# Optimization experiments

Measured on AMD Instinct MI355X. Metric: run time of the kernel, lower is better.

## Reference

```python
import jax, jax.numpy as jnp
import numpy as np

N, E, D, A = 50000, 1_600_000, 32, 2
H1, C1, H2, C2 = 4, 16, 2, 32  # GATv2Conv(D,16,heads=4) -> 64; GATv2Conv(64,32,heads=2) -> 64


def setup_inputs() -> dict:
    key = jax.random.key(0)
    ks = jax.random.split(key, 16)

    def glorot(k, shape):
        fan = shape[0] + shape[-1]
        return jax.random.normal(k, shape, jnp.float32) * np.float32(np.sqrt(2.0 / fan))

    return {
        "x": jax.random.normal(ks[0], (N, D), jnp.float32),
        "edge_index": jax.random.randint(ks[1], (2, E), 0, N),
        "edge_attr": jax.random.normal(ks[2], (E, 2), jnp.float32),
        # GATv2 layer 1 (lin_l/lin_r with bias, lin_edge no bias, att [H,C], out bias)
        "w1_l": glorot(ks[3], (D, H1 * C1)), "b1_l": jnp.zeros((H1 * C1,), jnp.float32),
        "w1_r": glorot(ks[4], (D, H1 * C1)), "b1_r": jnp.zeros((H1 * C1,), jnp.float32),
        "w1_e": glorot(ks[5], (2, H1 * C1)),
        "att1": glorot(ks[6], (H1, C1)),
        "bias1": jnp.zeros((H1 * C1,), jnp.float32),
        # GATv2 layer 2
        "w2_l": glorot(ks[7], (H1 * C1, H2 * C2)), "b2_l": jnp.zeros((H2 * C2,), jnp.float32),
        "w2_r": glorot(ks[8], (H1 * C1, H2 * C2)), "b2_r": jnp.zeros((H2 * C2,), jnp.float32),
        "w2_e": glorot(ks[9], (2, H2 * C2)),
        "att2": glorot(ks[10], (H2, C2)),
        "bias2": jnp.zeros((H2 * C2,), jnp.float32),
        # heads
        "w_actor": glorot(ks[11], (H2 * C2, A)), "b_actor": jnp.zeros((A,), jnp.float32),
        "w_critic": glorot(ks[12], (H2 * C2, 1)), "b_critic": jnp.zeros((1,), jnp.float32),
        "log_std": jnp.zeros((A,), jnp.float32),
    }


def _gatv2(x, src, dst, eattr, Wl, bl, Wr, br, We, att, bias, H, C, n):
    # PyG GATv2Conv: message j->i with i = dst, j = src
    xl = (x @ Wl + bl).reshape(n, H, C)  # source-side transform (x_j)
    xr = (x @ Wr + br).reshape(n, H, C)  # target-side transform (x_i)
    ee = (eattr @ We).reshape(-1, H, C)  # per-edge embedding
    z = jax.nn.leaky_relu(xl[src] + xr[dst] + ee, 0.2)  # [Etot, H, C]
    logits = jnp.einsum('ehc,hc->eh', z, att)  # [Etot, H]
    # segment softmax over incoming edges of each dst node
    m = jax.ops.segment_max(logits, dst, num_segments=n)
    p = jnp.exp(logits - m[dst])
    denom = jax.ops.segment_sum(p, dst, num_segments=n)
    alpha = p / denom[dst]  # every node has a self-loop -> denom > 0
    msg = xl[src] * alpha[:, :, None]  # [Etot, H, C]
    out = jax.ops.segment_sum(msg, dst, num_segments=n)
    return out.reshape(n, H * C) + bias


def reference(x, edge_index, edge_attr,
              w1_l, b1_l, w1_r, b1_r, w1_e, att1, bias1,
              w2_l, b2_l, w2_r, b2_r, w2_e, att2, bias2,
              w_actor, b_actor, w_critic, b_critic, log_std):
    src, dst = edge_index[0], edge_index[1]
    # add_self_loops=True, fill_value='mean': self-loop edge_attr = mean of incoming edge_attr
    cnt = jax.ops.segment_sum(jnp.ones((edge_attr.shape[0],), x.dtype), dst, num_segments=N)
    sums = jax.ops.segment_sum(edge_attr, dst, num_segments=N)
    loop_attr = sums / jnp.maximum(cnt, 1.0)[:, None]
    loop = jnp.arange(N, dtype=src.dtype)
    src_f = jnp.concatenate([src, loop])
    dst_f = jnp.concatenate([dst, loop])
    ea = jnp.concatenate([edge_attr, loop_attr], axis=0)

    h = jax.nn.relu(_gatv2(x, src_f, dst_f, ea, w1_l, b1_l, w1_r, b1_r, w1_e, att1, bias1, H1, C1, N))
    h = jax.nn.relu(_gatv2(h, src_f, dst_f, ea, w2_l, b2_l, w2_r, b2_r, w2_e, att2, bias2, H2, C2, N))

    action_mean = jnp.tanh(h @ w_actor + b_actor)  # [N, A]
    value = h @ w_critic + b_critic               # [N, 1]
    std = jnp.exp(log_std)                        # [A]  (Normal(action_mean, std))
    return action_mean, std, value
```

## Files before the change

### kernel.cpp

```cpp
#include <hip/hip_runtime.h>
#include <hip/hip_fp16.h>
#include <math.h>

#define DIN   32
#define F1    64
#define F2    64

typedef _Float16 h2 __attribute__((ext_vector_type(2)));

template <class T, class F>
__device__ __forceinline__ T bitc(F f) { return __builtin_bit_cast(T, f); }

__device__ __forceinline__ unsigned f16pack(float a, float b) {
    h2 h = { (_Float16)a, (_Float16)b };
    return bitc<unsigned>(h);
}

template <int K>
__device__ __forceinline__ void lin_lr_body(int bid,
        const float* __restrict__ x,
        const float* __restrict__ Wl, const float* __restrict__ bl,
        const float* __restrict__ Wr, const float* __restrict__ br,
        __half* __restrict__ xl, float* __restrict__ xr, int n) {
    __shared__ float Ash[32][K + 4];
    __shared__ float Wsh[K][128];
    const int t = threadIdx.x;
    const int node0 = bid * 32;

    for (int idx = t; idx < 32 * (K / 4); idx += 256) {
        int m = idx / (K / 4), kq = idx % (K / 4);
        float4 v = make_float4(0.f, 0.f, 0.f, 0.f);
        if (node0 + m < n) v = ((const float4*)(x + (size_t)(node0 + m) * K))[kq];
        *(float4*)&Ash[m][kq * 4] = v;
    }
    for (int idx = t; idx < K * 32; idx += 256) {
        int k = idx / 32, j4 = idx % 32;
        float4 v = (j4 < 16) ? ((const float4*)(Wl + (size_t)k * 64))[j4]
                             : ((const float4*)(Wr + (size_t)k * 64))[j4 - 16];
        *(float4*)&Wsh[k][j4 * 4] = v;
    }
    __syncthreads();

    const int ty = t >> 4;
    const int tx = t & 15;
    float acc0[8], acc1[8];
#pragma unroll
    for (int j = 0; j < 8; j++) { acc0[j] = 0.f; acc1[j] = 0.f; }

#pragma unroll 4
    for (int k = 0; k < K; k++) {
        float a0 = Ash[ty * 2 + 0][k];
        float a1 = Ash[ty * 2 + 1][k];
        float4 w0 = *(const float4*)&Wsh[k][tx * 8];
        float4 w1 = *(const float4*)&Wsh[k][tx * 8 + 4];
        acc0[0] += a0 * w0.x; acc0[1] += a0 * w0.y;
        acc0[2] += a0 * w0.z; acc0[3] += a0 * w0.w;
        acc0[4] += a0 * w1.x; acc0[5] += a0 * w1.y;
        acc0[6] += a0 * w1.z; acc0[7] += a0 * w1.w;
        acc1[0] += a1 * w0.x; acc1[1] += a1 * w0.y;
        acc1[2] += a1 * w0.z; acc1[3] += a1 * w0.w;
        acc1[4] += a1 * w1.x; acc1[5] += a1 * w1.y;
        acc1[6] += a1 * w1.z; acc1[7] += a1 * w1.w;
    }

    const float* bsrc = (tx < 8) ? bl : br;
    int jb = (tx < 8) ? tx * 8 : (tx - 8) * 8;
    float4 b0 = ((const float4*)(bsrc + jb))[0];
    float4 b1 = ((const float4*)(bsrc + jb))[1];
#pragma unroll
    for (int m = 0; m < 2; m++) {
        int node = node0 + ty * 2 + m;
        if (node >= n) continue;
        const float* ac = (m == 0) ? acc0 : acc1;
        float o0 = ac[0] + b0.x, o1 = ac[1] + b0.y;
        float o2 = ac[2] + b0.z, o3 = ac[3] + b0.w;
        float o4 = ac[4] + b1.x, o5 = ac[5] + b1.y;
        float o6 = ac[6] + b1.z, o7 = ac[7] + b1.w;
        if (tx < 8) {
            uint4 pk;
            pk.x = f16pack(o0, o1); pk.y = f16pack(o2, o3);
            pk.z = f16pack(o4, o5); pk.w = f16pack(o6, o7);
            *((uint4*)(xl + (size_t)node * 64 + jb)) = pk;
        } else {
            ((float4*)(xr + (size_t)node * 64 + jb))[0] = make_float4(o0, o1, o2, o3);
            ((float4*)(xr + (size_t)node * 64 + jb))[1] = make_float4(o4, o5, o6, o7);
        }
    }
}

__global__ __launch_bounds__(256, 2)
void fused_bcount_lin1(const int* __restrict__ dstr, int* __restrict__ cursor,
                       int* __restrict__ chunkoff, int* __restrict__ rank,
                       int E, int Ec, int NB, int gridLin,
                       const float* __restrict__ x,
                       const float* __restrict__ Wl, const float* __restrict__ bl,
                       const float* __restrict__ Wr, const float* __restrict__ br,
                       __half* __restrict__ xl, float* __restrict__ xr, int n) {
    __shared__ int hist[256];
    if ((int)blockIdx.x < gridLin) {
        lin_lr_body<DIN>(blockIdx.x, x, Wl, bl, Wr, br, xl, xr, n);
        return;
    }
    const int blk = blockIdx.x - gridLin;
    const int t = threadIdx.x;
    hist[t] = 0;
    __syncthreads();
    const int s0 = blk * Ec, s1 = min(E, s0 + Ec);
    for (int e = s0 + t; e < s1; e += 256)
        rank[e] = atomicAdd(&hist[dstr[e] >> 8], 1);
    __syncthreads();
    if (t < NB) {
        int h = hist[t];
        chunkoff[blk * 256 + t] = h ? atomicAdd(&cursor[t], h) : 0;
    }
}

__global__ __launch_bounds__(512)
void scatter_buckets(const int* __restrict__ srcr, const int* __restrict__ dstr,
                     const float* __restrict__ ea, const int* __restrict__ rank,
                     const int* __restrict__ chunkoff,
                     int2* __restrict__ inter, int E, int Ec, int NB, int cap) {
    __shared__ int colsh[256];
    const int blk = blockIdx.x;
    const int t = threadIdx.x;
    if (t < 256) colsh[t] = (t < NB) ? (t * cap + chunkoff[blk * 256 + t]) : 0;
    __syncthreads();
    const int s0 = blk * Ec, s1 = min(E, s0 + Ec);
    for (int e = s0 + t; e < s1; e += 512) {
        int d = dstr[e];
        float2 v = ((const float2*)ea)[e];
        int2 r;
        r.x = srcr[e] | ((d & 255) << 24);
        r.y = (int)f16pack(v.x, v.y);
        inter[colsh[d >> 8] + rank[e]] = r;
    }
}

__global__ __launch_bounds__(512)
void bucket_csr(const int2* __restrict__ inter, const int* __restrict__ cursor,
                int2* __restrict__ rse, float2* __restrict__ la2,
                int2* __restrict__ edges, int NB, int N, int cap) {
    __shared__ int sh[256];
    __shared__ int cur[256];
    const int b = blockIdx.x, t = threadIdx.x;
    const int bstart = b * cap;
    const int bend = bstart + cursor[b];

    if (t < 256) sh[t] = 0;
    __syncthreads();
    for (int pos = bstart + t; pos < bend; pos += 512)
        atomicAdd(&sh[((unsigned)inter[pos].x) >> 24], 1);
    __syncthreads();
    int cnt_v = 0, myrs = 0;
    if (t < 256) cnt_v = sh[t];
    __syncthreads();
    if (t < 256) sh[t] = cnt_v;
    __syncthreads();
    for (int off = 1; off < 256; off <<= 1) {
        int x = (t >= off && t < 256) ? sh[t - off] : 0;
        __syncthreads();
        if (t < 256) sh[t] += x;
        __syncthreads();
    }
    if (t < 256) {
        int excl = sh[t] - cnt_v;
        cur[t] = excl;
        myrs = bstart + excl;
        int node = b * 256 + t;
        if (node < N) rse[node] = make_int2(myrs, myrs + cnt_v);
    }
    __syncthreads();
    for (int pos = bstart + t; pos < bend; pos += 512) {
        int2 r = inter[pos];
        int k = atomicAdd(&cur[((unsigned)r.x) >> 24], 1);
        r.x &= 0x00FFFFFF;
        edges[bstart + k] = r;
    }
    int zend = (b + 1) * cap + ((b == NB - 1) ? 64 : 0);
    for (int pos = bend + t; pos < zend; pos += 512)
        edges[pos] = make_int2(0, 0);
    __syncthreads();
    if (t < 256) {
        int node = b * 256 + t;
        if (node < N) {
            float s0 = 0.f, s1 = 0.f;
            for (int pos = myrs; pos < myrs + cnt_v; pos++) {
                unsigned u = (unsigned)edges[pos].y;
                s0 += (float)bitc<_Float16>((unsigned short)(u & 0xFFFFu));
                s1 += (float)bitc<_Float16>((unsigned short)(u >> 16));
            }
            float inv = cnt_v ? 1.0f / (float)cnt_v : 0.f;
            la2[node] = make_float2(s0 * inv, s1 * inv);
        }
    }
}

__global__ __launch_bounds__(256, 2)
void lin_lr_tiled64(const float* __restrict__ x,
                    const float* __restrict__ Wl, const float* __restrict__ bl,
                    const float* __restrict__ Wr, const float* __restrict__ br,
                    __half* __restrict__ xl, float* __restrict__ xr, int n) {
    lin_lr_body<F1>(blockIdx.x, x, Wl, bl, Wr, br, xl, xr, n);
}

template <int H, int C, bool FUSE_HEADS>
__global__ __launch_bounds__(256)
void gat_kernel(const __half* __restrict__ xl, const float* __restrict__ xr,
                const int2* __restrict__ rse, const float2* __restrict__ la2,
                const int2* __restrict__ edges,
                const float* __restrict__ We, const float* __restrict__ att,
                const float* __restrict__ bias, float* __restrict__ hout,
                const float* __restrict__ wa, const float* __restrict__ ba,
                const float* __restrict__ wc, const float* __restrict__ bcv,
                const float* __restrict__ ls, float* __restrict__ pout,
                int n) {
    constexpr int LPH = C / 4;
    if (FUSE_HEADS && blockIdx.x == 0 && threadIdx.x < 2)
        pout[(size_t)n * 2 + threadIdx.x] = expf(ls[threadIdx.x]);
    const int lane = threadIdx.x & 63;
    const int wid = (blockIdx.x * blockDim.x + threadIdx.x) >> 6;
    if (wid >= n) return;
    const int i = wid;
    const int g = lane >> 4;
    const int q = lane & 15;

    const uint2* xlh = (const uint2*)xl;
    const float4 xri = ((const float4*)(xr + (size_t)i * 64))[q];
    const float4 we0 = ((const float4*)We)[q];
    const float4 we1 = ((const float4*)(We + 64))[q];
    float4 av = ((const float4*)att)[q];
    const float LOG2E = 1.4426950408889634f;
    av.x *= LOG2E; av.y *= LOG2E; av.z *= LOG2E; av.w *= LOG2E;

    const h2 xrih01 = { (_Float16)xri.x, (_Float16)xri.y };
    const h2 xrih23 = { (_Float16)xri.z, (_Float16)xri.w };
    const h2 we0h01 = { (_Float16)we0.x, (_Float16)we0.y };
    const h2 we0h23 = { (_Float16)we0.z, (_Float16)we0.w };
    const h2 we1h01 = { (_Float16)we1.x, (_Float16)we1.y };
    const h2 we1h23 = { (_Float16)we1.z, (_Float16)we1.w };
    const h2 avh01  = { (_Float16)av.x, (_Float16)av.y };
    const h2 avh23  = { (_Float16)av.z, (_Float16)av.w };
    const h2 lk = { (_Float16)0.2f, (_Float16)0.2f };

    float den = 0.f;
    float a0 = 0.f, a1 = 0.f, a2 = 0.f, a3 = 0.f;

    const int2 se = rse[i];
    const int e0 = se.x, e1 = se.y;
    const int r = (e1 - e0) & 7;

    auto edge_logit = [&](unsigned eabits, uint2 xp, float2& f01, float2& f23) -> float {
        h2 ea0h = bitc<h2>((eabits & 0xFFFFu) | (eabits << 16));
        h2 ea1h = bitc<h2>((eabits >> 16) | (eabits & 0xFFFF0000u));
        h2 xv01 = bitc<h2>(xp.x), xv23 = bitc<h2>(xp.y);
        h2 z01 = xv01 + (ea0h * we0h01 + (ea1h * we1h01 + xrih01));
        h2 z23 = xv23 + (ea0h * we0h23 + (ea1h * we1h23 + xrih23));
        z01 = __builtin_elementwise_max(z01, z01 * lk);
        z23 = __builtin_elementwise_max(z23, z23 * lk);
        f01 = make_float2((float)xv01[0], (float)xv01[1]);
        f23 = make_float2((float)xv23[0], (float)xv23[1]);
        return __builtin_amdgcn_fdot2(z01, avh01,
               __builtin_amdgcn_fdot2(z23, avh23, 0.f, false), false);
    };

    if (r) {
        int2 h0 = edges[e0 + g];
        int2 h1 = edges[e0 + 4 + g];
        uint2 xp0 = xlh[(h0.x << 4) + q];
        uint2 xp1 = xlh[(h1.x << 4) + q];
        const bool v0 = g < r;
        const bool v1 = (4 + g) < r;
        float2 f001, f023, f101, f123;
        float l0 = edge_logit((unsigned)h0.y, xp0, f001, f023);
        float l1 = edge_logit((unsigned)h1.y, xp1, f101, f123);
#pragma unroll
        for (int m = 1; m < LPH; m <<= 1) {
            l0 += __shfl_xor(l0, m, 64);
            l1 += __shfl_xor(l1, m, 64);
        }
        float p0 = v0 ? exp2f(l0) : 0.f;
        float p1 = v1 ? exp2f(l1) : 0.f;
        den += p0 + p1;
        a0 = fmaf(p0, f001.x, fmaf(p1, f101.x, a0));
        a1 = fmaf(p0, f001.y, fmaf(p1, f101.y, a1));
        a2 = fmaf(p0, f023.x, fmaf(p1, f123.x, a2));
        a3 = fmaf(p0, f023.y, fmaf(p1, f123.y, a3));
    }

    const int em = e0 + r;
    int2 rn0 = edges[em + g];
    int2 rn1 = edges[em + 4 + g];
    uint2 xpn0 = xlh[(rn0.x << 4) + q];
    uint2 xpn1 = xlh[(rn1.x << 4) + q];

    for (int eb = em; eb < e1; eb += 8) {
        int2 r0 = rn0, r1 = rn1;
        uint2 xp0 = xpn0, xp1 = xpn1;
        rn0 = edges[eb + 8 + g];
        rn1 = edges[eb + 12 + g];
        xpn0 = xlh[(rn0.x << 4) + q];
        xpn1 = xlh[(rn1.x << 4) + q];

        float2 f001, f023, f101, f123;
        float l0 = edge_logit((unsigned)r0.y, xp0, f001, f023);
        float l1 = edge_logit((unsigned)r1.y, xp1, f101, f123);
#pragma unroll
        for (int m = 1; m < LPH; m <<= 1) {
            l0 += __shfl_xor(l0, m, 64);
            l1 += __shfl_xor(l1, m, 64);
        }
        float p0 = exp2f(l0);
        float p1 = exp2f(l1);
        den += p0 + p1;
        a0 = fmaf(p0, f001.x, fmaf(p1, f101.x, a0));
        a1 = fmaf(p0, f001.y, fmaf(p1, f101.y, a1));
        a2 = fmaf(p0, f023.x, fmaf(p1, f123.x, a2));
        a3 = fmaf(p0, f023.y, fmaf(p1, f123.y, a3));
    }

#pragma unroll
    for (int m = 16; m < 64; m <<= 1) {
        den += __shfl_xor(den, m, 64);
        a0 += __shfl_xor(a0, m, 64);
        a1 += __shfl_xor(a1, m, 64);
        a2 += __shfl_xor(a2, m, 64);
        a3 += __shfl_xor(a3, m, 64);
    }

    const float2 lam = la2[i];
    uint2 xpi = xlh[(i << 4) + q];
    h2 xi01 = bitc<h2>(xpi.x), xi23 = bitc<h2>(xpi.y);
    float4 xlv = make_float4((float)xi01[0], (float)xi01[1],
                             (float)xi23[0], (float)xi23[1]);
    {
        float z0 = xlv.x + fmaf(lam.x, we0.x, fmaf(lam.y, we1.x, xri.x));
        float z1 = xlv.y + fmaf(lam.x, we0.y, fmaf(lam.y, we1.y, xri.y));
        float z2 = xlv.z + fmaf(lam.x, we0.z, fmaf(lam.y, we1.z, xri.z));
        float z3 = xlv.w + fmaf(lam.x, we0.w, fmaf(lam.y, we1.w, xri.w));
        z0 = fmaxf(z0, 0.2f * z0);
        z1 = fmaxf(z1, 0.2f * z1);
        z2 = fmaxf(z2, 0.2f * z2);
        z3 = fmaxf(z3, 0.2f * z3);
        float l = fmaf(z0, av.x, fmaf(z1, av.y, fmaf(z2, av.z, z3 * av.w)));
#pragma unroll
        for (int m = 1; m < LPH; m <<= 1) l += __shfl_xor(l, m, 64);
        float p = exp2f(l);
        den += p;
        a0 = fmaf(p, xlv.x, a0);
        a1 = fmaf(p, xlv.y, a1);
        a2 = fmaf(p, xlv.z, a2);
        a3 = fmaf(p, xlv.w, a3);
    }

    float rd = 1.0f / den;
    const float4 bv = ((const float4*)bias)[q];
    float4 o;
    o.x = fmaxf(fmaf(a0, rd, bv.x), 0.f);
    o.y = fmaxf(fmaf(a1, rd, bv.y), 0.f);
    o.z = fmaxf(fmaf(a2, rd, bv.z), 0.f);
    o.w = fmaxf(fmaf(a3, rd, bv.w), 0.f);

    if (!FUSE_HEADS) {
        if (g == 0) ((float4*)(hout + (size_t)i * 64))[q] = o;
    } else {
        float4 wa01 = ((const float4*)wa)[q * 2];
        float4 wa23 = ((const float4*)wa)[q * 2 + 1];
        float4 wcv  = ((const float4*)wc)[q];
        float d0 = o.x * wa01.x + o.y * wa01.z + o.z * wa23.x + o.w * wa23.z;
        float d1 = o.x * wa01.y + o.y * wa01.w + o.z * wa23.y + o.w * wa23.w;
        float d2 = o.x * wcv.x + o.y * wcv.y + o.z * wcv.z + o.w * wcv.w;
#pragma unroll
        for (int m = 1; m < 16; m <<= 1) {
            d0 += __shfl_xor(d0, m, 64);
            d1 += __shfl_xor(d1, m, 64);
            d2 += __shfl_xor(d2, m, 64);
        }
        if (lane == 0) {
            pout[(size_t)i * 2 + 0] = tanhf(d0 + ba[0]);
            pout[(size_t)i * 2 + 1] = tanhf(d1 + ba[1]);
            pout[(size_t)n * 2 + 2 + i] = d2 + bcv[0];
        }
    }
}


extern "C" void kernel_launch(void* const* d_in, const int* in_sizes, int n_in,
                              void* d_out, int out_size, void* d_ws, size_t ws_size,
                              hipStream_t stream) {
    const float* x    = (const float*)d_in[0];
    const int*   ei   = (const int*)  d_in[1];
    const float* ea   = (const float*)d_in[2];
    const float* w1l  = (const float*)d_in[3];
    const float* b1l  = (const float*)d_in[4];
    const float* w1r  = (const float*)d_in[5];
    const float* b1r  = (const float*)d_in[6];
    const float* w1e  = (const float*)d_in[7];
    const float* att1 = (const float*)d_in[8];
    const float* bias1= (const float*)d_in[9];
    const float* w2l  = (const float*)d_in[10];
    const float* b2l  = (const float*)d_in[11];
    const float* w2r  = (const float*)d_in[12];
    const float* b2r  = (const float*)d_in[13];
    const float* w2e  = (const float*)d_in[14];
    const float* att2 = (const float*)d_in[15];
    const float* bias2= (const float*)d_in[16];
    const float* wa   = (const float*)d_in[17];
    const float* ba   = (const float*)d_in[18];
    const float* wc   = (const float*)d_in[19];
    const float* bcv  = (const float*)d_in[20];
    const float* ls   = (const float*)d_in[21];

    const int N = in_sizes[0] / DIN;
    const int E = in_sizes[2] / 2;
    const int* srcr = ei;
    const int* dstr = ei + E;

    const int NB = (N + 255) >> 8;
    const int Ec = (E + 255) / 256;
    int cap = (E + NB - 1) / NB;
    cap = ((cap + cap / 4) + 63) & ~63;

    char* p = (char*)d_ws;
    auto alloc = [&](size_t bytes) -> void* {
        void* r = (void*)p;
        p += (bytes + 255) & ~(size_t)255;
        return r;
    };
    int*    cursor   = (int*)   alloc(256 * 4);
    int*    chunkoff = (int*)   alloc(256 * 256 * 4);
    int*    rank     = (int*)   alloc((size_t)E * 4);
    int2*   rse      = (int2*)  alloc((size_t)N * 8);
    float2* la2      = (float2*)alloc((size_t)N * 8);
    int2*   edges    = (int2*)  alloc(((size_t)NB * cap + 64) * 8);
    __half* xl       = (__half*)alloc((size_t)N * F1 * 2);
    float*  xr       = (float*) alloc((size_t)N * F1 * 4);
    float*  h1       = (float*) alloc((size_t)N * F1 * 4);
    float*  h2buf    = (float*) alloc((size_t)N * F2 * 4);
    int2* inter = (int2*)h1;
    (void)ws_size; (void)n_in; (void)out_size;

    (void)hipMemsetAsync(cursor, 0, 256 * 4, stream);

    const int TB = 256;
    int gridGemm = (N + 31) / 32;
    int gridWave = (N + 3) / 4;

    fused_bcount_lin1<<<gridGemm + 256, TB, 0, stream>>>(
        dstr, cursor, chunkoff, rank, E, Ec, NB, gridGemm,
        x, w1l, b1l, w1r, b1r, xl, xr, N);
    scatter_buckets<<<256, 512, 0, stream>>>(srcr, dstr, ea, rank, chunkoff,
                                             inter, E, Ec, NB, cap);
    bucket_csr<<<NB, 512, 0, stream>>>(inter, cursor, rse, la2, edges, NB, N, cap);

    gat_kernel<4, 16, false><<<gridWave, TB, 0, stream>>>(
        xl, xr, rse, la2, edges, w1e, att1, bias1, h1,
        nullptr, nullptr, nullptr, nullptr, nullptr, nullptr, N);
    lin_lr_tiled64<<<gridGemm, TB, 0, stream>>>(h1, w2l, b2l, w2r, b2r, xl, xr, N);
    gat_kernel<2, 32, true><<<gridWave, TB, 0, stream>>>(
        xl, xr, rse, la2, edges, w2e, att2, bias2, h2buf,
        wa, ba, wc, bcv, ls, (float*)d_out, N);
}
```

Measured before the change: 300.2 us.

## Fuse bucket scatter into count kernel and deepen edge prefetch pipeline

Merges the bucket-scatter pass into the bucket-count kernel. Each chunk block now counts, reserves a base offset in each bucket, then recomputes local ranks with a second shared-memory atomic pass. This removes the per-edge rank array, the chunkoff array and one kernel launch, but dstr is read twice, and the order of edges within a bucket becomes nondeterministic. Separately, the GAT edge loop prefetches edge records two iterations ahead instead of one, so more gather latency is hidden at the cost of extra registers.

After: 304.5 us. Within noise of the previous version (+1.4%).

```diff
diff --git a/kernel.cpp b/kernel.cpp
--- a/kernel.cpp
+++ b/kernel.cpp
@@ -89,14 +89,16 @@
 }
 
 __global__ __launch_bounds__(256, 2)
-void fused_bcount_lin1(const int* __restrict__ dstr, int* __restrict__ cursor,
-                       int* __restrict__ chunkoff, int* __restrict__ rank,
-                       int E, int Ec, int NB, int gridLin,
-                       const float* __restrict__ x,
-                       const float* __restrict__ Wl, const float* __restrict__ bl,
-                       const float* __restrict__ Wr, const float* __restrict__ br,
-                       __half* __restrict__ xl, float* __restrict__ xr, int n) {
+void fused_csr_lin1(const int* __restrict__ dstr, const int* __restrict__ srcr,
+                    const float* __restrict__ ea, int* __restrict__ cursor,
+                    int2* __restrict__ inter,
+                    int E, int Ec, int NB, int cap, int gridLin,
+                    const float* __restrict__ x,
+                    const float* __restrict__ Wl, const float* __restrict__ bl,
+                    const float* __restrict__ Wr, const float* __restrict__ br,
+                    __half* __restrict__ xl, float* __restrict__ xr, int n) {
     __shared__ int hist[256];
+    __shared__ int base[256];
     if ((int)blockIdx.x < gridLin) {
         lin_lr_body<DIN>(blockIdx.x, x, Wl, bl, Wr, br, xl, xr, n);
         return;
@@ -107,32 +109,24 @@
     __syncthreads();
     const int s0 = blk * Ec, s1 = min(E, s0 + Ec);
     for (int e = s0 + t; e < s1; e += 256)
-        rank[e] = atomicAdd(&hist[dstr[e] >> 8], 1);
+        atomicAdd(&hist[dstr[e] >> 8], 1);
     __syncthreads();
     if (t < NB) {
         int h = hist[t];
-        chunkoff[blk * 256 + t] = h ? atomicAdd(&cursor[t], h) : 0;
-    }
-}
-
-__global__ __launch_bounds__(512)
-void scatter_buckets(const int* __restrict__ srcr, const int* __restrict__ dstr,
-                     const float* __restrict__ ea, const int* __restrict__ rank,
-                     const int* __restrict__ chunkoff,
-                     int2* __restrict__ inter, int E, int Ec, int NB, int cap) {
-    __shared__ int colsh[256];
-    const int blk = blockIdx.x;
-    const int t = threadIdx.x;
-    if (t < 256) colsh[t] = (t < NB) ? (t * cap + chunkoff[blk * 256 + t]) : 0;
-    __syncthreads();
-    const int s0 = blk * Ec, s1 = min(E, s0 + Ec);
-    for (int e = s0 + t; e < s1; e += 512) {
+        base[t] = t * cap + (h ? atomicAdd(&cursor[t], h) : 0);
+    }
+    __syncthreads();
+    hist[t] = 0;
+    __syncthreads();
+    for (int e = s0 + t; e < s1; e += 256) {
         int d = dstr[e];
+        int b = d >> 8;
+        int lr = atomicAdd(&hist[b], 1);
         float2 v = ((const float2*)ea)[e];
         int2 r;
         r.x = srcr[e] | ((d & 255) << 24);
         r.y = (int)f16pack(v.x, v.y);
-        inter[colsh[d >> 8] + rank[e]] = r;
+        inter[base[b] + lr] = r;
     }
 }
 
@@ -288,22 +282,25 @@
     }
 
     const int em = e0 + r;
-    int2 rn0 = edges[em + g];
-    int2 rn1 = edges[em + 4 + g];
-    uint2 xpn0 = xlh[(rn0.x << 4) + q];
-    uint2 xpn1 = xlh[(rn1.x << 4) + q];
+    int2 ra0 = edges[em + g];
+    int2 ra1 = edges[em + 4 + g];
+    uint2 xa0 = xlh[(ra0.x << 4) + q];
+    uint2 xa1 = xlh[(ra1.x << 4) + q];
+    int2 rb0 = edges[em + 8 + g];
+    int2 rb1 = edges[em + 12 + g];
 
     for (int eb = em; eb < e1; eb += 8) {
-        int2 r0 = rn0, r1 = rn1;
-        uint2 xp0 = xpn0, xp1 = xpn1;
-        rn0 = edges[eb + 8 + g];
-        rn1 = edges[eb + 12 + g];
-        xpn0 = xlh[(rn0.x << 4) + q];
-        xpn1 = xlh[(rn1.x << 4) + q];
+        int2 rc0 = ra0, rc1 = ra1;
+        uint2 xc0 = xa0, xc1 = xa1;
+        ra0 = rb0; ra1 = rb1;
+        xa0 = xlh[(ra0.x << 4) + q];
+        xa1 = xlh[(ra1.x << 4) + q];
+        rb0 = edges[eb + 16 + g];
+        rb1 = edges[eb + 20 + g];
 
         float2 f001, f023, f101, f123;
-        float l0 = edge_logit((unsigned)r0.y, xp0, f001, f023);
-        float l1 = edge_logit((unsigned)r1.y, xp1, f101, f123);
+        float l0 = edge_logit((unsigned)rc0.y, xc0, f001, f023);
+        float l1 = edge_logit((unsigned)rc1.y, xc1, f101, f123);
 #pragma unroll
         for (int m = 1; m < LPH; m <<= 1) {
             l0 += __shfl_xor(l0, m, 64);
@@ -427,8 +424,6 @@
         return r;
     };
     int*    cursor   = (int*)   alloc(256 * 4);
-    int*    chunkoff = (int*)   alloc(256 * 256 * 4);
-    int*    rank     = (int*)   alloc((size_t)E * 4);
     int2*   rse      = (int2*)  alloc((size_t)N * 8);
     float2* la2      = (float2*)alloc((size_t)N * 8);
     int2*   edges    = (int2*)  alloc(((size_t)NB * cap + 64) * 8);
@@ -445,11 +440,9 @@
     int gridGemm = (N + 31) / 32;
     int gridWave = (N + 3) / 4;
 
-    fused_bcount_lin1<<<gridGemm + 256, TB, 0, stream>>>(
-        dstr, cursor, chunkoff, rank, E, Ec, NB, gridGemm,
+    fused_csr_lin1<<<gridGemm + 256, TB, 0, stream>>>(
+        dstr, srcr, ea, cursor, inter, E, Ec, NB, cap, gridGemm,
         x, w1l, b1l, w1r, b1r, xl, xr, N);
-    scatter_buckets<<<256, 512, 0, stream>>>(srcr, dstr, ea, rank, chunkoff,
-                                             inter, E, Ec, NB, cap);
     bucket_csr<<<NB, 512, 0, stream>>>(inter, cursor, rse, la2, edges, NB, N, cap);
 
     gat_kernel<4, 16, false><<<gridWave, TB, 0, stream>>>(
```
